# Optimization experiments

Measured on AMD Instinct MI355X. Metric: run time of the kernel, lower is better.

The kernel has to match this reference:

```python
import jax, jax.numpy as jnp
import numpy as np

B, T, D, HD = 4, 4096, 1024, 64

def setup_inputs() -> dict:
    key = jax.random.key(0)
    kx, kq, kk, kv = jax.random.split(key, 4)
    s = 1.0 / np.sqrt(D)
    return {
        "x": jax.random.normal(kx, (B, T, D), dtype=jnp.float32),
        "wq": jax.random.uniform(kq, (HD, D), jnp.float32, -s, s),
        "wk": jax.random.uniform(kk, (HD, D), jnp.float32, -s, s),
        "wv": jax.random.uniform(kv, (HD, D), jnp.float32, -s, s),
    }

def reference(x, wq, wk, wv):
    # Linear(D, headDim, bias=False): y = x @ W.T with W of shape [headDim, D]
    Q = jnp.einsum('btD,dD->btd', x, wq)
    K = jnp.einsum('bsD,dD->bsd', x, wk)
    V = jnp.einsum('bsD,dD->bsd', x, wv)
    head_dim = wq.shape[0]
    logits = jnp.einsum('btd,bsd->bts', Q, K) / jnp.sqrt(jnp.float32(head_dim))
    attn = jax.nn.softmax(logits, axis=-1)
    return jnp.einsum('bts,bsd->btd', attn, V)
```

## Files before the change

kernel.cpp:

```cpp
#include <hip/hip_runtime.h>
#include <math.h>

#define TLEN 4096
#define BD   1024
#define HDIM 64
#define NB   4

typedef __attribute__((ext_vector_type(8))) short bf16x8;
typedef __attribute__((ext_vector_type(4))) float f32x4;
typedef __attribute__((ext_vector_type(16))) float f32x16;

typedef const __attribute__((address_space(1))) unsigned char* gp_t;
typedef __attribute__((address_space(3))) unsigned char* lp_t;

__device__ __forceinline__ void async_cp16(const void* g, void* l) {
    __builtin_amdgcn_global_load_lds((gp_t)g, (lp_t)l, 16, 0, 0);
}

__device__ __forceinline__ unsigned short f2bf(float f) {
    union { float f; unsigned u; } v; v.f = f;
    unsigned r = v.u + 0x7FFF + ((v.u >> 16) & 1);
    return (unsigned short)(r >> 16);
}

__device__ __forceinline__ unsigned cvt_pk_bf16(float lo, float hi) {
    unsigned r;
    asm("v_cvt_pk_bf16_f32 %0, %1, %2" : "=v"(r) : "v"(lo), "v"(hi));
    return r;
}

__device__ __forceinline__ bf16x8 cvt8pk(const float4 a, const float4 b) {
    union { unsigned u[4]; bf16x8 v; } r;
    r.u[0] = cvt_pk_bf16(a.x, a.y);
    r.u[1] = cvt_pk_bf16(a.z, a.w);
    r.u[2] = cvt_pk_bf16(b.x, b.y);
    r.u[3] = cvt_pk_bf16(b.z, b.w);
    return r.v;
}

__global__ __launch_bounds__(256) void wconv_kernel(
    const float* __restrict__ wq, const float* __restrict__ wk,
    const float* __restrict__ wv, unsigned short* __restrict__ wbf)
{
    const int r = blockIdx.x;
    const float* src = (r < 64) ? wq : (r < 128) ? wk : wv;
    const int rr = r & 63;
    const int c  = threadIdx.x * 4;
    float4 a = *(const float4*)&src[(size_t)rr * BD + c];
    uint2 o;
    o.x = cvt_pk_bf16(a.x, a.y);
    o.y = cvt_pk_bf16(a.z, a.w);
    *(uint2*)&wbf[(size_t)r * BD + c] = o;
}

__global__ __launch_bounds__(256, 2) void qkv_kernel(
    const float* __restrict__ x,
    const unsigned short* __restrict__ wbf,
    unsigned short* __restrict__ Qb,
    unsigned short* __restrict__ Kb,
    unsigned short* __restrict__ Vt)
{
    const int r0   = blockIdx.x * 32;
    const int tid  = threadIdx.x;
    const int lane = tid & 63;
    const int w    = tid >> 6;
    const int g    = lane >> 4;
    const int c    = lane & 15;

    __shared__ __align__(16) float          xf[2][32 * 64];
    __shared__ __align__(16) unsigned short vtr[64][40];

    int wrow[3];
    #pragma unroll
    for (int t = 0; t < 3; ++t) wrow[t] = (w * 3 + t) * 16 + c;

    f32x4 acc[3][2];
    #pragma unroll
    for (int t = 0; t < 3; ++t)
        #pragma unroll
        for (int rg = 0; rg < 2; ++rg) acc[t][rg] = (f32x4){0.f, 0.f, 0.f, 0.f};

    uint4 wfA[6], wfB[6];

    #define LOAD_WF(W, k0s)                                                     \
        {                                                                       \
            _Pragma("unroll")                                                   \
            for (int t = 0; t < 3; ++t)                                         \
                _Pragma("unroll")                                               \
                for (int h = 0; h < 2; ++h)                                     \
                    W[t * 2 + h] = *(const uint4*)                              \
                        &wbf[(size_t)wrow[t] * BD + (k0s) + (h * 4 + g) * 8];   \
        }
    #define STAGE_X(buf, k0s)                                                   \
        {                                                                       \
            _Pragma("unroll")                                                   \
            for (int ii = 0; ii < 2; ++ii) {                                    \
                const int L   = ii * 256 + tid;                                 \
                const int row = L >> 4;                                         \
                const int gch = (L & 15) ^ (row & 15);                          \
                async_cp16(&x[(size_t)(r0 + row) * BD + (k0s) + gch * 4],       \
                           &xf[buf][L * 4]);                                    \
            }                                                                   \
        }

    #define QKV_BODY(itv, cbv, WCUR, WNXT)                                      \
        {                                                                       \
            __syncthreads();                          \
            if ((itv) < 15) {                                                   \
                STAGE_X((cbv) ^ 1, ((itv) + 1) * 64)                            \
                LOAD_WF(WNXT, ((itv) + 1) * 64)                                 \
            }                                                                   \
            _Pragma("unroll")                                                   \
            for (int h = 0; h < 2; ++h) {                                       \
                const int oct = h * 4 + g;                                      \
                bf16x8 aX[2];                                                   \
                _Pragma("unroll")                                               \
                for (int rg = 0; rg < 2; ++rg) {                                \
                    const int row = rg * 16 + c;                                \
                    const float4 a0 = *(const float4*)                          \
                        &xf[cbv][row * 64 + ((2 * oct) ^ c) * 4];               \
                    const float4 a1 = *(const float4*)                          \
                        &xf[cbv][row * 64 + ((2 * oct + 1) ^ c) * 4];           \
                    aX[rg] = cvt8pk(a0, a1);                                    \
                }                                                               \
                _Pragma("unroll")                                               \
                for (int t = 0; t < 3; ++t) {                                   \
                    const bf16x8 bW = *(const bf16x8*)&WCUR[t * 2 + h];         \
                    _Pragma("unroll")                                           \
                    for (int rg = 0; rg < 2; ++rg)                              \
                        acc[t][rg] = __builtin_amdgcn_mfma_f32_16x16x32_bf16(   \
                            aX[rg], bW, acc[t][rg], 0, 0, 0);                   \
                }                                                               \
            }                                                                   \
        }

    LOAD_WF(wfA, 0)
    STAGE_X(0, 0)

    #pragma unroll
    for (int it2 = 0; it2 < 8; ++it2) {
        QKV_BODY(2 * it2,     0, wfA, wfB)
        QKV_BODY(2 * it2 + 1, 1, wfB, wfA)
    }

    const float qscale = 0.18033688f;
    const int   bb     = r0 / TLEN;
    const int   trow   = r0 % TLEN;
    #pragma unroll
    for (int t = 0; t < 3; ++t) {
        const int m = w * 3 + t;
        #pragma unroll
        for (int rg = 0; rg < 2; ++rg)
            #pragma unroll
            for (int i = 0; i < 4; ++i) {
                const int row = rg * 16 + g * 4 + i;
                if (m < 4)
                    Qb[(size_t)(r0 + row) * HDIM + m * 16 + c]
                        = f2bf(acc[t][rg][i] * qscale);
                else if (m < 8)
                    Kb[(size_t)(r0 + row) * HDIM + (m - 4) * 16 + c]
                        = f2bf(acc[t][rg][i]);
                else
                    vtr[(m - 8) * 16 + c][row] = f2bf(acc[t][rg][i]);
            }
    }
    __syncthreads();
    {
        const int d    = tid >> 2;
        const int part = tid & 3;
        uint4 v0 = *(const uint4*)&vtr[d][part * 8];
        unsigned short* dst = Vt + (size_t)bb * HDIM * TLEN + (size_t)d * TLEN
                            + trow + part * 8;
        *(uint4*)&dst[0] = v0;
    }
    #undef LOAD_WF
    #undef STAGE_X
    #undef QKV_BODY
}

template <int KEYS>
__global__ __launch_bounds__(256, 2) void attn_kernel(
    const unsigned short* __restrict__ Qb,
    const unsigned short* __restrict__ Kb,
    const unsigned short* __restrict__ Vt,
    float* __restrict__ O1, float* __restrict__ Ml, float* __restrict__ out)
{
    const int b     = blockIdx.y;
    const int q0    = blockIdx.x * 128;
    const int split = blockIdx.z;
    const int sbase = split * KEYS;

    const unsigned short* Qp = Qb + (size_t)b * TLEN * HDIM;
    const unsigned short* Kp = Kb + (size_t)b * TLEN * HDIM + (size_t)sbase * HDIM;
    const unsigned short* Vp = Vt + (size_t)b * HDIM * TLEN + sbase;

    const int tid  = threadIdx.x;
    const int lane = tid & 63;
    const int w    = tid >> 6;
    const int ql   = lane & 31;
    const int hi   = lane >> 5;
    const int ch   = lane & 7;

    __shared__ __align__(16) unsigned short ksh[2][4096];
    __shared__ __align__(16) unsigned short vsh[2][4096];

    bf16x8 qB[4];
    #pragma unroll
    for (int s = 0; s < 4; ++s)
        qB[s] = *(const bf16x8*)
            &Qp[(size_t)(q0 + w * 32 + ql) * HDIM + s * 16 + hi * 8];

    float  lsum = 0.f;
    f32x16 oacc[2];
    #pragma unroll
    for (int dt = 0; dt < 2; ++dt)
        #pragma unroll
        for (int i = 0; i < 16; ++i) oacc[dt][i] = 0.f;

    const int nt = KEYS / 64;

    uint4 kreg[2], vreg[2];
    #define LOAD_KV(s0)                                                         \
        {                                                                       \
            _Pragma("unroll")                                                   \
            for (int ii = 0; ii < 2; ++ii) {                                    \
                const int L   = ii * 256 + tid;                                 \
                const int row = L >> 3;                                         \
                const int jl  = (L & 7) ^ (row & 7);                            \
                kreg[ii] = *(const uint4*)&Kp[(size_t)((s0) + row) * HDIM + jl * 8]; \
                vreg[ii] = *(const uint4*)&Vp[(size_t)row * TLEN + (s0) + jl * 8];   \
            }                                                                   \
        }
    #define WRITE_KV(buf)                                                       \
        {                                                                       \
            _Pragma("unroll")                                                   \
            for (int ii = 0; ii < 2; ++ii) {                                    \
                const int L = ii * 256 + tid;                                   \
                *(uint4*)&ksh[buf][L * 8] = kreg[ii];                           \
                *(uint4*)&vsh[buf][L * 8] = vreg[ii];                           \
            }                                                                   \
        }

    LOAD_KV(0)
    WRITE_KV(0)

    for (int it = 0; it < nt; ++it) {
        const int cb = it & 1;
        __syncthreads();

        if (it + 1 < nt) LOAD_KV((it + 1) * 64)

        f32x16 sacc[2];
        #pragma unroll
        for (int kt = 0; kt < 2; ++kt)
            #pragma unroll
            for (int i = 0; i < 16; ++i) sacc[kt][i] = 0.f;
        __builtin_amdgcn_s_setprio(1);
        #pragma unroll
        for (int kt = 0; kt < 2; ++kt)
            #pragma unroll
            for (int s = 0; s < 4; ++s) {
                const bf16x8 kA = *(const bf16x8*)
                    &ksh[cb][(32 * kt + ql) * 64 + ((2 * s + hi) ^ ch) * 8];
                sacc[kt] = __builtin_amdgcn_mfma_f32_32x32x16_bf16(
                    kA, qB[s], sacc[kt], 0, 0, 0);
            }
        __builtin_amdgcn_s_setprio(0);

        if (it + 1 < nt) WRITE_KV(cb ^ 1)

        bf16x8 paf[4];
        #pragma unroll
        for (int kt = 0; kt < 2; ++kt) {
            float p[16];
            #pragma unroll
            for (int i = 0; i < 16; ++i)
                p[i] = __builtin_amdgcn_exp2f(sacc[kt][i]);
            lsum += (((p[0] + p[1]) + (p[2] + p[3]))
                   + ((p[4] + p[5]) + (p[6] + p[7])))
                  + (((p[8] + p[9]) + (p[10] + p[11]))
                   + ((p[12] + p[13]) + (p[14] + p[15])));
            #pragma unroll
            for (int bb = 0; bb < 2; ++bb) {
                const unsigned X0 = cvt_pk_bf16(p[8 * bb + 0], p[8 * bb + 1]);
                const unsigned X1 = cvt_pk_bf16(p[8 * bb + 2], p[8 * bb + 3]);
                const unsigned Z0 = cvt_pk_bf16(p[8 * bb + 4], p[8 * bb + 5]);
                const unsigned Z1 = cvt_pk_bf16(p[8 * bb + 6], p[8 * bb + 7]);
                auto s02 = __builtin_amdgcn_permlane32_swap(X0, Z0, false, false);
                auto s13 = __builtin_amdgcn_permlane32_swap(X1, Z1, false, false);
                union { unsigned u[4]; bf16x8 v; } pu;
                pu.u[0] = s02[0]; pu.u[1] = s13[0];
                pu.u[2] = s02[1]; pu.u[3] = s13[1];
                paf[kt * 2 + bb] = pu.v;
            }
        }

        __builtin_amdgcn_s_setprio(1);
        #pragma unroll
        for (int dt = 0; dt < 2; ++dt)
            #pragma unroll
            for (int s = 0; s < 4; ++s) {
                const bf16x8 vB = *(const bf16x8*)
                    &vsh[cb][(32 * dt + ql) * 64 + ((2 * s + hi) ^ ch) * 8];
                oacc[dt] = __builtin_amdgcn_mfma_f32_32x32x16_bf16(
                    paf[s], vB, oacc[dt], 0, 0, 0);
            }
        __builtin_amdgcn_s_setprio(0);
    }
    #undef LOAD_KV
    #undef WRITE_KV

    lsum += __shfl_xor(lsum, 32);

    if (KEYS == TLEN) {
        #pragma unroll
        for (int r = 0; r < 16; ++r) {
            const int   qr   = (r & 3) + 8 * (r >> 2) + 4 * hi;
            const float inv  = 1.0f / __shfl(lsum, qr);
            const size_t orow = (size_t)b * TLEN + q0 + w * 32 + qr;
            out[orow * HDIM + ql]      = oacc[0][r] * inv;
            out[orow * HDIM + 32 + ql] = oacc[1][r] * inv;
        }
    } else {
        float* Od = (split == 0)
            ? out : O1 + (size_t)(split - 1) * NB * TLEN * HDIM;
        #pragma unroll
        for (int r = 0; r < 16; ++r) {
            const int   qr   = (r & 3) + 8 * (r >> 2) + 4 * hi;
            const size_t orow = (size_t)b * TLEN + q0 + w * 32 + qr;
            Od[orow * HDIM + ql]      = oacc[0][r];
            Od[orow * HDIM + 32 + ql] = oacc[1][r];
        }
        if (lane < 32)
            Ml[(size_t)(split * NB + b) * TLEN + q0 + w * 32 + lane] = lsum;
    }
}

__global__ __launch_bounds__(256) void merge_kernel(
    float* __restrict__ out, const float* __restrict__ O1,
    const float* __restrict__ Ml)
{
    const int idx  = blockIdx.x * 256 + threadIdx.x;
    const int row  = idx >> 4;
    const int col4 = (idx & 15) * 4;
    const int b    = row >> 12;
    const int t    = row & (TLEN - 1);
    float l = 0.f;
    #pragma unroll
    for (int s = 0; s < 4; ++s) l += Ml[(size_t)(s * NB + b) * TLEN + t];
    const float inv = 1.0f / l;
    float4 a = *(const float4*)&out[(size_t)row * HDIM + col4];
    #pragma unroll
    for (int s = 1; s < 4; ++s) {
        float4 p = *(const float4*)
            &O1[(size_t)(s - 1) * NB * TLEN * HDIM + (size_t)row * HDIM + col4];
        a.x += p.x; a.y += p.y; a.z += p.z; a.w += p.w;
    }
    a.x *= inv; a.y *= inv; a.z *= inv; a.w *= inv;
    *(float4*)&out[(size_t)row * HDIM + col4] = a;
}

extern "C" void kernel_launch(void* const* d_in, const int* in_sizes, int n_in,
                              void* d_out, int out_size, void* d_ws, size_t ws_size,
                              hipStream_t stream)
{
    (void)in_sizes; (void)n_in; (void)out_size;
    const float* x  = (const float*)d_in[0];
    const float* wq = (const float*)d_in[1];
    const float* wk = (const float*)d_in[2];
    const float* wv = (const float*)d_in[3];
    float* out = (float*)d_out;

    unsigned short* wbf = (unsigned short*)d_out;
    unsigned short* Qbf = (unsigned short*)d_ws;
    unsigned short* Kbf = Qbf + (size_t)NB * TLEN * HDIM;
    unsigned short* Vtb = Kbf + (size_t)NB * TLEN * HDIM;
    float* Ml = (float*)((char*)d_ws + (size_t)3 * NB * TLEN * HDIM * 2);
    float* O1 = Ml + (size_t)4 * NB * TLEN;
    const size_t ws_need = (size_t)3 * NB * TLEN * HDIM * 2
                         + (size_t)4 * NB * TLEN * 4
                         + (size_t)3 * NB * TLEN * HDIM * 4;
    const bool use_split = ws_size >= ws_need;

    wconv_kernel<<<dim3(192), 256, 0, stream>>>(wq, wk, wv, wbf);
    qkv_kernel<<<dim3(NB * TLEN / 32), 256, 0, stream>>>(x, wbf, Qbf, Kbf, Vtb);

    if (use_split) {
        attn_kernel<TLEN / 4><<<dim3(TLEN / 128, NB, 4), 256, 0, stream>>>(
            Qbf, Kbf, Vtb, O1, Ml, out);
        merge_kernel<<<dim3(NB * TLEN * 16 / 256), 256, 0, stream>>>(out, O1, Ml);
    } else {
        attn_kernel<TLEN><<<dim3(TLEN / 128, NB, 1), 256, 0, stream>>>(
            Qbf, Kbf, Vtb, O1, Ml, out);
    }
}
```

Measured before the change: 151.9 us.

## Stage QKV weights and x through LDS with two-deep register prefetch

The QKV projection kernel no longer uses async global-to-LDS copies for x or per-thread global loads of weight fragments. It now loads the whole 192x64 weight tile and x tile into registers two iterations ahead, writes them to double-buffered swizzled LDS after the MFMA work, and reads weight fragments from LDS. The attention kernel also moves its K/V LDS write to the end of the iteration so the loads have more time to land. This trades extra LDS capacity and registers (which may reduce occupancy) for fewer redundant weight loads and deeper latency hiding.

```diff
diff --git a/kernel.cpp b/kernel.cpp
--- a/kernel.cpp
+++ b/kernel.cpp
@@ -9,13 +9,6 @@
 typedef __attribute__((ext_vector_type(8))) short bf16x8;
 typedef __attribute__((ext_vector_type(4))) float f32x4;
 typedef __attribute__((ext_vector_type(16))) float f32x16;
-
-typedef const __attribute__((address_space(1))) unsigned char* gp_t;
-typedef __attribute__((address_space(3))) unsigned char* lp_t;
-
-__device__ __forceinline__ void async_cp16(const void* g, void* l) {
-    __builtin_amdgcn_global_load_lds((gp_t)g, (lp_t)l, 16, 0, 0);
-}
 
 __device__ __forceinline__ unsigned short f2bf(float f) {
     union { float f; unsigned u; } v; v.f = f;
@@ -67,53 +60,66 @@
     const int g    = lane >> 4;
     const int c    = lane & 15;
 
+    __shared__ __align__(16) unsigned short wsh[2][192 * 64];
     __shared__ __align__(16) float          xf[2][32 * 64];
     __shared__ __align__(16) unsigned short vtr[64][40];
 
-    int wrow[3];
-    #pragma unroll
-    for (int t = 0; t < 3; ++t) wrow[t] = (w * 3 + t) * 16 + c;
-
     f32x4 acc[3][2];
     #pragma unroll
     for (int t = 0; t < 3; ++t)
         #pragma unroll
         for (int rg = 0; rg < 2; ++rg) acc[t][rg] = (f32x4){0.f, 0.f, 0.f, 0.f};
 
-    uint4 wfA[6], wfB[6];
-
-    #define LOAD_WF(W, k0s)                                                     \
-        {                                                                       \
-            _Pragma("unroll")                                                   \
-            for (int t = 0; t < 3; ++t)                                         \
-                _Pragma("unroll")                                               \
-                for (int h = 0; h < 2; ++h)                                     \
-                    W[t * 2 + h] = *(const uint4*)                              \
-                        &wbf[(size_t)wrow[t] * BD + (k0s) + (h * 4 + g) * 8];   \
-        }
-    #define STAGE_X(buf, k0s)                                                   \
+    uint4 wrg[2][6], xrg[2][2];
+
+    #define LOAD_W2(P, k0s)                                                     \
+        {                                                                       \
+            _Pragma("unroll")                                                   \
+            for (int ii = 0; ii < 6; ++ii) {                                    \
+                const int L   = ii * 256 + tid;                                 \
+                const int row = L >> 3;                                         \
+                const int jl  = (L & 7) ^ (row & 7);                            \
+                wrg[P][ii] = *(const uint4*)&wbf[(size_t)row * BD + (k0s) + jl * 8]; \
+            }                                                                   \
+        }
+    #define WRITE_W2(P)                                                         \
+        {                                                                       \
+            _Pragma("unroll")                                                   \
+            for (int ii = 0; ii < 6; ++ii) {                                    \
+                const int L = ii * 256 + tid;                                   \
+                *(uint4*)&wsh[P][L * 8] = wrg[P][ii];                           \
+            }                                                                   \
+        }
+    #define LOAD_X2(P, k0s)                                                     \
         {                                                                       \
             _Pragma("unroll")                                                   \
             for (int ii = 0; ii < 2; ++ii) {                                    \
                 const int L   = ii * 256 + tid;                                 \
                 const int row = L >> 4;                                         \
                 const int gch = (L & 15) ^ (row & 15);                          \
-                async_cp16(&x[(size_t)(r0 + row) * BD + (k0s) + gch * 4],       \
-                           &xf[buf][L * 4]);                                    \
-            }                                                                   \
-        }
-
-    #define QKV_BODY(itv, cbv, WCUR, WNXT)                                      \
-        {                                                                       \
-            __syncthreads();                          \
-            if ((itv) < 15) {                                                   \
-                STAGE_X((cbv) ^ 1, ((itv) + 1) * 64)                            \
-                LOAD_WF(WNXT, ((itv) + 1) * 64)                                 \
+                xrg[P][ii] = *(const uint4*)&x[(size_t)(r0 + row) * BD + (k0s) + gch * 4]; \
+            }                                                                   \
+        }
+    #define WRITE_X2(P)                                                         \
+        {                                                                       \
+            _Pragma("unroll")                                                   \
+            for (int ii = 0; ii < 2; ++ii) {                                    \
+                const int L = ii * 256 + tid;                                   \
+                *(uint4*)&xf[P][L * 4] = xrg[P][ii];                            \
+            }                                                                   \
+        }
+
+    #define QKV_BODY(itv, cbv, PW)                                              \
+        {                                                                       \
+            __syncthreads();                               \
+            if ((itv) < 14) {                                                   \
+                LOAD_W2(cbv, ((itv) + 2) * 64)    \
+                LOAD_X2(cbv, ((itv) + 2) * 64)                                  \
             }                                                                   \
             _Pragma("unroll")                                                   \
             for (int h = 0; h < 2; ++h) {                                       \
                 const int oct = h * 4 + g;                                      \
-                bf16x8 aX[2];                                                   \
+                bf16x8 aX[2], bW[3];                                            \
                 _Pragma("unroll")                                               \
                 for (int rg = 0; rg < 2; ++rg) {                                \
                     const int row = rg * 16 + c;                                \
@@ -124,23 +130,34 @@
                     aX[rg] = cvt8pk(a0, a1);                                    \
                 }                                                               \
                 _Pragma("unroll")                                               \
-                for (int t = 0; t < 3; ++t) {                                   \
-                    const bf16x8 bW = *(const bf16x8*)&WCUR[t * 2 + h];         \
+                for (int t = 0; t < 3; ++t)                                     \
+                    bW[t] = *(const bf16x8*)                                    \
+                        &wsh[cbv][((w * 3 + t) * 16 + c) * 64                   \
+                                  + ((oct ^ (c & 7)) * 8)];                     \
+                _Pragma("unroll")                                               \
+                for (int t = 0; t < 3; ++t)                                     \
                     _Pragma("unroll")                                           \
                     for (int rg = 0; rg < 2; ++rg)                              \
                         acc[t][rg] = __builtin_amdgcn_mfma_f32_16x16x32_bf16(   \
-                            aX[rg], bW, acc[t][rg], 0, 0, 0);                   \
-                }                                                               \
-            }                                                                   \
-        }
-
-    LOAD_WF(wfA, 0)
-    STAGE_X(0, 0)
+                            aX[rg], bW[t], acc[t][rg], 0, 0, 0);                \
+            }                                                                   \
+            if ((itv) < 15) {                                                   \
+                WRITE_W2(PW)              \
+                WRITE_X2(PW)                                                    \
+            }                                                                   \
+        }
+
+    LOAD_W2(0, 0)
+    LOAD_X2(0, 0)
+    WRITE_W2(0)
+    WRITE_X2(0)
+    LOAD_W2(1, 64)
+    LOAD_X2(1, 64)
 
     #pragma unroll
     for (int it2 = 0; it2 < 8; ++it2) {
-        QKV_BODY(2 * it2,     0, wfA, wfB)
-        QKV_BODY(2 * it2 + 1, 1, wfB, wfA)
+        QKV_BODY(2 * it2,     0, 1)
+        QKV_BODY(2 * it2 + 1, 1, 0)
     }
 
     const float qscale = 0.18033688f;
@@ -173,8 +190,10 @@
                             + trow + part * 8;
         *(uint4*)&dst[0] = v0;
     }
-    #undef LOAD_WF
-    #undef STAGE_X
+    #undef LOAD_W2
+    #undef WRITE_W2
+    #undef LOAD_X2
+    #undef WRITE_X2
     #undef QKV_BODY
 }
 
@@ -266,8 +285,6 @@
                     kA, qB[s], sacc[kt], 0, 0, 0);
             }
         __builtin_amdgcn_s_setprio(0);
-
-        if (it + 1 < nt) WRITE_KV(cb ^ 1)
 
         bf16x8 paf[4];
         #pragma unroll
@@ -306,6 +323,8 @@
                     paf[s], vB, oacc[dt], 0, 0, 0);
             }
         __builtin_amdgcn_s_setprio(0);
+
+        if (it + 1 < nt) WRITE_KV(cb ^ 1)
     }
     #undef LOAD_KV
     #undef WRITE_KV
```

After: 221.9 us. +46.0%, slower.
